# Performance work log

Hardware: AMD Instinct MI355X
Metric: run time of the kernel (lower is better)

## Reference

```python
import jax, jax.numpy as jnp
import numpy as np

LN_EPS = 1e-5  # torch.nn.LayerNorm default

def g(x):
    # minGRU activation: x + 0.5 for x >= 0, sigmoid(x) otherwise (always positive)
    return jnp.where(x >= 0, x + 0.5, jax.nn.sigmoid(x))

def log_g(x):
    return jnp.where(x >= 0, jnp.log(jax.nn.relu(x) + 0.5), -jax.nn.softplus(-x))

def layernorm(x, gamma, beta):
    mu = jnp.mean(x, axis=-1, keepdims=True)
    var = jnp.var(x, axis=-1, keepdims=True)
    return (x - mu) * jax.lax.rsqrt(var + LN_EPS) * gamma + beta

def mingru_scan(gate, hidden, h0):
    # gate, hidden: (B,S,D); h0: (B,1,D) positive
    # z = sigmoid(gate); h_t = (1-z_t)*h_{t-1} + z_t * g(hidden_t)
    # evaluated via Heinsen parallel scan in log space
    log_z = -jax.nn.softplus(-gate)          # log sigmoid(gate)
    log_coeffs = -jax.nn.softplus(gate)      # log(1 - sigmoid(gate))
    log_h0 = jnp.log(h0)                     # (B,1,D)
    log_tilde_h = log_g(hidden)
    a_star = jnp.cumsum(
        jnp.concatenate([jnp.zeros_like(log_h0), log_coeffs], axis=1), axis=1
    )                                        # (B,S+1,D)
    log_vals = jnp.concatenate([log_h0, log_z + log_tilde_h], axis=1) - a_star
    log_h = a_star + jax.lax.cumlogsumexp(log_vals, axis=1)
    return jnp.exp(log_h)[:, 1:]             # (B,S,D)

def setup_inputs() -> dict:
    key = jax.random.key(0)
    k1, k2 = jax.random.split(key)
    B, S, D, L = 8, 4096, 1024, 3
    x = jax.random.normal(k1, (B, S, D), dtype=jnp.float32)
    W = jax.random.normal(k2, (L, D, 2 * D), dtype=jnp.float32) * 0.02
    b = jnp.zeros((L, 2 * D), dtype=jnp.float32)
    ln_gamma = jnp.ones((L, D), dtype=jnp.float32)
    ln_beta = jnp.zeros((L, D), dtype=jnp.float32)
    return {"x": x, "ln_gamma": ln_gamma, "ln_beta": ln_beta, "W": W, "b": b}

def reference(x, ln_gamma, ln_beta, W, b):
    B, S, D = x.shape
    L = W.shape[0]
    inp = x
    next_hidden = []
    for l in range(L):
        h_prev = jnp.full((B, 1, D), 0.5, dtype=x.dtype)  # g(zeros) = 0.5
        xn = layernorm(inp, ln_gamma[l], ln_beta[l])
        gh = jnp.einsum('bsd,de->bse', xn, W[l]) + b[l]   # (B,S,2D)
        gate, hidden = jnp.split(gh, 2, axis=2)
        out = mingru_scan(gate, hidden, h_prev)
        next_hidden.append(out[:, -1:])
        out = out + inp  # residual (sizes equal -> identity res_align)
        inp = out
    return (out, *next_hidden)
```

## Files before the change

### kernel.cpp

```cpp
#include <hip/hip_runtime.h>

typedef unsigned short u16;
typedef unsigned int   u32;
typedef float  f32x2  __attribute__((ext_vector_type(2)));
typedef float  f32x4  __attribute__((ext_vector_type(4)));
typedef short  bf16x8 __attribute__((ext_vector_type(8)));
typedef u16    u16x4  __attribute__((ext_vector_type(4)));
typedef u32    u32x4  __attribute__((ext_vector_type(4)));

#define BQ 8
#define SQ 4096
#define DQ 1024
#define NQ 2048
#define MQ 32768
#define KQ 1024
#define CCH 64
#define TCH 64
#define NT 16

__device__ __forceinline__ float bf2f(u16 u){
  union { u32 i; float f; } v; v.i = ((u32)u) << 16; return v.f;
}
__device__ __forceinline__ u16 f2bf(float f){
  union { float f; u32 i; } v; v.f = f;
  u32 r = v.i + 0x7fffu + ((v.i >> 16) & 1u);
  return (u16)(r >> 16);
}

__device__ __forceinline__ void sig_ab(float gate, float hid, float& a, float& bv){
  float eg = __expf(gate);
  float a_ = __builtin_amdgcn_rcpf(1.f + eg);
  float z  = 1.f - a_;
  float eh = __expf(hid);
  float sg = eh * __builtin_amdgcn_rcpf(1.f + eh);
  float gval = (hid >= 0.f) ? (hid + 0.5f) : sg;
  a = a_; bv = z * gval;
}

__device__ __forceinline__ void gload_lds16(const u16* g, u16* l){
  __builtin_amdgcn_global_load_lds(
      (const __attribute__((address_space(1))) u32*)g,
      (__attribute__((address_space(3)))       u32*)l,
      16, 0, 0);
}

__global__ __launch_bounds__(256) void wt_cast(const float* __restrict__ W,
                                               u16* __restrict__ WT){
  __shared__ float t[64][65];
  const int l  = blockIdx.z;
  const int k0 = blockIdx.x << 6, n0 = blockIdx.y << 6;
  const float* Wl = W  + (size_t)l * KQ * NQ;
  u16*         Tl = WT + (size_t)l * NQ * KQ;
  const int c = threadIdx.x & 63, r4 = threadIdx.x >> 6;
  #pragma unroll
  for (int i = 0; i < 16; ++i){
    int r = i * 4 + r4;
    t[r][c] = Wl[(size_t)(k0 + r) * NQ + n0 + c];
  }
  __syncthreads();
  #pragma unroll
  for (int i = 0; i < 16; ++i){
    int r = i * 4 + r4;
    Tl[(size_t)(n0 + r) * KQ + k0 + c] = f2bf(t[c][r]);
  }
}

__global__ __launch_bounds__(256) void ln_cast(const float* __restrict__ x,
                                               const float* __restrict__ gamma,
                                               const float* __restrict__ beta,
                                               u16* __restrict__ xn){
  const size_t row = blockIdx.x;
  const int tid = threadIdx.x;
  f32x4 xv = *(const f32x4*)(x + row * DQ + tid * 4);
  float s  = xv[0] + xv[1] + xv[2] + xv[3];
  float s2 = xv[0]*xv[0] + xv[1]*xv[1] + xv[2]*xv[2] + xv[3]*xv[3];
  #pragma unroll
  for (int off = 32; off > 0; off >>= 1){
    s  += __shfl_down(s,  off);
    s2 += __shfl_down(s2, off);
  }
  __shared__ float red[8];
  const int wave = tid >> 6, lane = tid & 63;
  if (lane == 0){ red[wave] = s; red[4 + wave] = s2; }
  __syncthreads();
  s  = red[0] + red[1] + red[2] + red[3];
  s2 = red[4] + red[5] + red[6] + red[7];
  const float mean = s * (1.f / DQ);
  float var = fmaxf(s2 * (1.f / DQ) - mean * mean, 0.f);
  const float rstd = rsqrtf(var + 1e-5f);
  f32x4 gv = *(const f32x4*)(gamma + tid * 4);
  f32x4 bv = *(const f32x4*)(beta  + tid * 4);
  u16x4 o;
  #pragma unroll
  for (int e = 0; e < 4; ++e) o[e] = f2bf((xv[e] - mean) * rstd * gv[e] + bv[e]);
  *(u16x4*)(xn + row * DQ + tid * 4) = o;
}

__global__ __launch_bounds__(512, 2) void gemm_k8(const u16* __restrict__ A,
                                                  const u16* __restrict__ Bt,
                                                  const float* __restrict__ bias,
                                                  u32* __restrict__ abv,
                                                  float* __restrict__ pq){
  __shared__ u16 lds[2][2][2][8192];
  const int bid = blockIdx.x;
  const int swz = ((bid & 7) << 7) | (bid >> 3);
  const int bn = swz & 7, bm = swz >> 3;
  const int m0 = bm << 8;
  const int tid = threadIdx.x;
  const int w = tid >> 6, lane = tid & 63;
  const int wr = w >> 2, wc = w & 3;
  const int lr = lane & 15, hi = lane >> 4;
  const int sl8 = lane >> 3;
  const int sslot = (lane & 7) ^ sl8;

  f32x4 acc[2][2][4][2] = {};
  bf16x8 afr[4][2];
  bf16x8 bf0[2][2], bf1[2][2];

#define FENCE asm volatile("" ::: "memory")
#define BAR do { FENCE; __builtin_amdgcn_s_barrier(); FENCE; } while(0)

#define STAGE(op, hf, kt, pb_) do {                                            \
    const u16* gsrc_ = (op) ? Bt : A;                                          \
    const int rb_ = (op) ? ((bn << 7) + (hf) * 1024) : (m0 + ((hf) << 7));     \
    _Pragma("unroll")                                                          \
    for (int g_ = 0; g_ < 2; ++g_){                                            \
      const int row_ = (w << 4) + (g_ << 3) + sl8;                             \
      gload_lds16(gsrc_ + (size_t)(rb_ + row_) * KQ + ((kt) << 6) + (sslot << 3),\
                  &lds[pb_][op][hf][((w << 4) + (g_ << 3)) << 6]);             \
    }                                                                          \
  } while(0)

#define LDSRD(dst, base_, row_, slot_) do {                                    \
    const int r_ = (row_);                                                     \
    dst = *(const bf16x8*)((const char*)(base_) +                              \
          ((r_ << 7) + ((((slot_)) ^ (r_ & 7)) << 4)));                        \
  } while(0)

#define RD_A(hf) do {                                                          \
    const u16* Ah_ = &lds[pb][0][hf][0];                                       \
    _Pragma("unroll")                                                          \
    for (int i_ = 0; i_ < 4; ++i_)                                             \
      _Pragma("unroll")                                                        \
      for (int kk_ = 0; kk_ < 2; ++kk_)                                        \
        LDSRD(afr[i_][kk_], Ah_, (wr << 6) + (i_ << 4) + lr, (kk_ << 2) + hi); \
  } while(0)

#define RD_B(dst, hf) do {                                                     \
    const u16* Bh_ = &lds[pb][1][hf][0];                                       \
    _Pragma("unroll")                                                          \
    for (int j_ = 0; j_ < 2; ++j_)                                             \
      _Pragma("unroll")                                                        \
      for (int kk_ = 0; kk_ < 2; ++kk_)                                        \
        LDSRD(dst[j_][kk_], Bh_, (wc << 5) + (j_ << 4) + lr, (kk_ << 2) + hi); \
  } while(0)

#define MM(qm, qn, B) do {                                                     \
    _Pragma("unroll")                                                          \
    for (int i_ = 0; i_ < 4; ++i_)                                             \
      _Pragma("unroll")                                                        \
      for (int j_ = 0; j_ < 2; ++j_)                                           \
        _Pragma("unroll")                                                      \
        for (int kk_ = 0; kk_ < 2; ++kk_)                                      \
          acc[qm][qn][i_][j_] = __builtin_amdgcn_mfma_f32_16x16x32_bf16(       \
              afr[i_][kk_], B[j_][kk_], acc[qm][qn][i_][j_], 0, 0, 0);         \
  } while(0)

#define PH(VMW, STG, RDS, MFMAS) do {                                          \
    VMW;                                                                       \
    BAR;                                                                       \
    STG;                                                                       \
    RDS;                                                                       \
    asm volatile("s_waitcnt lgkmcnt(0)" ::: "memory");                         \
    __builtin_amdgcn_s_setprio(1);                                             \
    MFMAS;                                                                     \
    __builtin_amdgcn_s_setprio(0);                                             \
  } while(0)

  STAGE(1, 0, 0, 0); STAGE(0, 0, 0, 0); STAGE(1, 1, 0, 0); STAGE(0, 1, 0, 0);

  for (int t = 0; t < NT; ++t){
    const int pb = t & 1, qb = pb ^ 1;
    const bool s = (t + 1 < NT);
    PH(asm volatile("s_waitcnt vmcnt(4)" ::: "memory"),
       if (s) STAGE(1, 0, t + 1, qb),
       RD_A(0); RD_B(bf0, 0),
       MM(0, 0, bf0));
    PH(if (s) { asm volatile("s_waitcnt vmcnt(4)" ::: "memory"); }
       else   { asm volatile("s_waitcnt vmcnt(2)" ::: "memory"); },
       if (s) STAGE(0, 0, t + 1, qb),
       RD_B(bf1, 1),
       MM(0, 1, bf1));
    PH(if (s) { asm volatile("s_waitcnt vmcnt(4)" ::: "memory"); }
       else   { asm volatile("s_waitcnt vmcnt(0)" ::: "memory"); },
       if (s) STAGE(1, 1, t + 1, qb),
       RD_A(1),
       MM(1, 0, bf0));
    PH(,
       if (s) STAGE(0, 1, t + 1, qb),
       ,
       MM(1, 1, bf1));
  }
#undef PH
#undef MM
#undef RD_B
#undef RD_A
#undef LDSRD
#undef STAGE

  const int dbase = (bn << 7) + (wc << 5) + lr;
  #pragma unroll
  for (int qm = 0; qm < 2; ++qm){
    const int row00 = m0 + (qm << 7) + (wr << 6);
    float chP[2] = {1.f, 1.f}, chQ[2] = {0.f, 0.f};
    #pragma unroll
    for (int i = 0; i < 4; ++i){
      float sgP[2] = {1.f, 1.f}, sgQ[2] = {0.f, 0.f};
      #pragma unroll
      for (int r = 0; r < 4; ++r){
        const int row = row00 + (i << 4) + (hi << 2) + r;
        #pragma unroll
        for (int j = 0; j < 2; ++j){
          const int d = dbase + (j << 4);
          float gate = acc[qm][0][i][j][r] + bias[d];
          float hid  = acc[qm][1][i][j][r] + bias[1024 + d];
          float a, bv; sig_ab(gate, hid, a, bv);
          const u16 ua = f2bf(a), ub = f2bf(bv);
          abv[(size_t)row * 1024 + d] = (u32)ua | ((u32)ub << 16);
          const float ar = bf2f(ua), br = bf2f(ub);
          sgQ[j] = ar * sgQ[j] + br;
          sgP[j] *= ar;
        }
      }
      #pragma unroll
      for (int j = 0; j < 2; ++j){
        float p = sgP[j], q = sgQ[j];
        float p1 = __shfl_up(p, 16), q1 = __shfl_up(q, 16);
        if (hi >= 1){ q = p * q1 + q; p = p * p1; }
        float p2 = __shfl_up(p, 32), q2 = __shfl_up(q, 32);
        if (hi >= 2){ q = p * q2 + q; p = p * p2; }
        chQ[j] = p * chQ[j] + q;
        chP[j] = p * chP[j];
      }
    }
    if (hi == 3){
      const int bq = row00 >> 12, cq = (row00 >> 6) & 63;
      #pragma unroll
      for (int j = 0; j < 2; ++j){
        const int d = dbase + (j << 4);
        f32x2 v; v[0] = chP[j]; v[1] = chQ[j];
        *(f32x2*)(pq + ((((size_t)(bq * CCH + cq)) << 10) + d) * 2) = v;
      }
    }
  }
#undef BAR
#undef FENCE
}

__global__ __launch_bounds__(256) void scan2(const float* __restrict__ pq,
                                             float* __restrict__ hst,
                                             float* __restrict__ hlast){
  const int idx = blockIdx.x * 256 + threadIdx.x;
  const int b = idx >> 10, d = idx & 1023;
  float h = 0.5f;
  for (int c = 0; c < CCH; ++c){
    const size_t o = ((size_t)(b * CCH + c) << 10) + d;
    hst[o] = h;
    f32x2 v = *(const f32x2*)(pq + o * 2);
    h = v[0] * h + v[1];
  }
  hlast[idx] = h;
}

template<int MODE>
__global__ __launch_bounds__(256) void scan3f(const u32* __restrict__ abv,
                                              const float* __restrict__ hst,
                                              const void* __restrict__ inp,
                                              void* __restrict__ outp,
                                              u16* __restrict__ xn,
                                              const float* __restrict__ gamma,
                                              const float* __restrict__ beta){
  const int b = blockIdx.x >> 6;
  const int c = blockIdx.x & 63;
  const int tid = threadIdx.x;
  const int d4 = tid << 2;
  const int wave = tid >> 6, lane = tid & 63;
  const size_t srow = (size_t)(b * SQ + c * TCH);
  const u32* base = abv + srow * 1024 + d4;
  const size_t o = ((size_t)blockIdx.x << 10) + d4;
  f32x4 h0v = *(const f32x4*)(hst + o);
  float h[4] = {h0v[0], h0v[1], h0v[2], h0v[3]};
  __shared__ float red[2][8];
  f32x4 gv = {}, bvv = {};
  if (MODE != 2){
    gv  = *(const f32x4*)(gamma + d4);
    bvv = *(const f32x4*)(beta  + d4);
  }
  for (int t = 0; t < TCH; ++t){
    u32x4 ab = *(const u32x4*)(base + (size_t)t * 1024);
    f32x4 iv;
    if (MODE == 0){
      iv = *(const f32x4*)((const float*)inp + (srow + t) * DQ + d4);
    } else {
      u16x4 ib = *(const u16x4*)((const u16*)inp + (srow + t) * DQ + d4);
      #pragma unroll
      for (int e = 0; e < 4; ++e) iv[e] = bf2f(ib[e]);
    }
    f32x4 ov;
    #pragma unroll
    for (int e = 0; e < 4; ++e){
      const float a  = bf2f((u16)(ab[e] & 0xffffu));
      const float bv = bf2f((u16)(ab[e] >> 16));
      h[e] = a * h[e] + bv;
      ov[e] = h[e] + iv[e];
    }
    if (MODE == 2){
      *(f32x4*)((float*)outp + (srow + t) * DQ + d4) = ov;
    } else {
      u16x4 ob;
      #pragma unroll
      for (int e = 0; e < 4; ++e) ob[e] = f2bf(ov[e]);
      *(u16x4*)((u16*)outp + (srow + t) * DQ + d4) = ob;
      float s  = ov[0] + ov[1] + ov[2] + ov[3];
      float s2 = ov[0]*ov[0] + ov[1]*ov[1] + ov[2]*ov[2] + ov[3]*ov[3];
      #pragma unroll
      for (int off = 32; off > 0; off >>= 1){
        s  += __shfl_down(s,  off);
        s2 += __shfl_down(s2, off);
      }
      const int rb = t & 1;
      if (lane == 0){ red[rb][wave] = s; red[rb][4 + wave] = s2; }
      __syncthreads();
      s  = red[rb][0] + red[rb][1] + red[rb][2] + red[rb][3];
      s2 = red[rb][4] + red[rb][5] + red[rb][6] + red[rb][7];
      const float mean = s * (1.f / DQ);
      float var = fmaxf(s2 * (1.f / DQ) - mean * mean, 0.f);
      const float rstd = rsqrtf(var + 1e-5f);
      u16x4 xo;
      #pragma unroll
      for (int e = 0; e < 4; ++e)
        xo[e] = f2bf((ov[e] - mean) * rstd * gv[e] + bvv[e]);
      *(u16x4*)(xn + (srow + t) * DQ + d4) = xo;
    }
  }
}

extern "C" void kernel_launch(void* const* d_in, const int* in_sizes, int n_in,
                              void* d_out, int out_size, void* d_ws, size_t ws_size,
                              hipStream_t stream) {
  const float* x     = (const float*)d_in[0];
  const float* gamma = (const float*)d_in[1];
  const float* beta  = (const float*)d_in[2];
  const float* W     = (const float*)d_in[3];
  const float* bias  = (const float*)d_in[4];
  float* out = (float*)d_out;

  char* ws = (char*)d_ws;
  const size_t ACT = (size_t)MQ * DQ * 4;
  u16*   bufA = (u16*)(ws);
  u16*   bufB = (u16*)(ws + ACT);
  u32*   abv  = (u32*)(ws + 2 * ACT);
  u16*   xn   = (u16*)(ws + 3 * ACT);
  u16*   WT   = (u16*)(ws + 3 * ACT + (size_t)MQ * DQ * 2);
  float* pq   = (float*)(ws + 3 * ACT + (size_t)MQ * DQ * 2 + (size_t)3 * NQ * KQ * 2);
  float* hst  = pq + (size_t)2 * BQ * CCH * DQ;

  wt_cast<<<dim3(KQ / 64, NQ / 64, 3), 256, 0, stream>>>(W, WT);

  const dim3 ggrid((NQ / 256) * (MQ / 256));
  ln_cast<<<MQ, 256, 0, stream>>>(x, gamma, beta, xn);
  gemm_k8<<<ggrid, 512, 0, stream>>>(xn, WT, bias, abv, pq);
  scan2<<<(BQ * DQ) / 256, 256, 0, stream>>>(pq, hst, out + (size_t)MQ * DQ);
  scan3f<0><<<BQ * CCH, 256, 0, stream>>>(abv, hst, x, bufA, xn,
                                          gamma + DQ, beta + DQ);
  gemm_k8<<<ggrid, 512, 0, stream>>>(xn, WT + (size_t)NQ * KQ, bias + NQ,
                                     abv, pq);
  scan2<<<(BQ * DQ) / 256, 256, 0, stream>>>(pq, hst,
                                             out + (size_t)MQ * DQ + BQ * DQ);
  scan3f<1><<<BQ * CCH, 256, 0, stream>>>(abv, hst, bufA, bufB, xn,
                                          gamma + 2 * DQ, beta + 2 * DQ);
  gemm_k8<<<ggrid, 512, 0, stream>>>(xn, WT + (size_t)2 * NQ * KQ, bias + 2 * NQ,
                                     abv, pq);
  scan2<<<(BQ * DQ) / 256, 256, 0, stream>>>(pq, hst,
                                             out + (size_t)MQ * DQ + 2 * BQ * DQ);
  scan3f<2><<<BQ * CCH, 256, 0, stream>>>(abv, hst, bufB, out, nullptr,
                                          nullptr, nullptr);
}
```

Measured before the change: 732.5 us.

## Software-pipeline LDS fragment reads with MFMA using double-buffered A registers

```diff
diff --git a/kernel.cpp b/kernel.cpp
--- a/kernel.cpp
+++ b/kernel.cpp
@@ -114,11 +114,12 @@
   const int sslot = (lane & 7) ^ sl8;
 
   f32x4 acc[2][2][4][2] = {};
-  bf16x8 afr[4][2];
+  bf16x8 afrA[4][2], afrB[4][2];
   bf16x8 bf0[2][2], bf1[2][2];
 
 #define FENCE asm volatile("" ::: "memory")
 #define BAR do { FENCE; __builtin_amdgcn_s_barrier(); FENCE; } while(0)
+#define SB  __builtin_amdgcn_sched_barrier(0)
 
 #define STAGE(op, hf, kt, pb_) do {                                            \
     const u16* gsrc_ = (op) ? Bt : A;                                          \
@@ -137,17 +138,17 @@
           ((r_ << 7) + ((((slot_)) ^ (r_ & 7)) << 4)));                        \
   } while(0)
 
-#define RD_A(hf) do {                                                          \
-    const u16* Ah_ = &lds[pb][0][hf][0];                                       \
+#define RD_A(dst, hf, buf_) do {                                               \
+    const u16* Ah_ = &lds[buf_][0][hf][0];                                     \
     _Pragma("unroll")                                                          \
     for (int i_ = 0; i_ < 4; ++i_)                                             \
       _Pragma("unroll")                                                        \
       for (int kk_ = 0; kk_ < 2; ++kk_)                                        \
-        LDSRD(afr[i_][kk_], Ah_, (wr << 6) + (i_ << 4) + lr, (kk_ << 2) + hi); \
-  } while(0)
-
-#define RD_B(dst, hf) do {                                                     \
-    const u16* Bh_ = &lds[pb][1][hf][0];                                       \
+        LDSRD(dst[i_][kk_], Ah_, (wr << 6) + (i_ << 4) + lr, (kk_ << 2) + hi); \
+  } while(0)
+
+#define RD_B(dst, hf, buf_) do {                                               \
+    const u16* Bh_ = &lds[buf_][1][hf][0];                                     \
     _Pragma("unroll")                                                          \
     for (int j_ = 0; j_ < 2; ++j_)                                             \
       _Pragma("unroll")                                                        \
@@ -155,7 +156,9 @@
         LDSRD(dst[j_][kk_], Bh_, (wc << 5) + (j_ << 4) + lr, (kk_ << 2) + hi); \
   } while(0)
 
-#define MM(qm, qn, B) do {                                                     \
+#define MM(qm, qn, AR, B) do {                                                 \
+    SB;                                                                        \
+    __builtin_amdgcn_s_setprio(1);                                             \
     _Pragma("unroll")                                                          \
     for (int i_ = 0; i_ < 4; ++i_)                                             \
       _Pragma("unroll")                                                        \
@@ -163,50 +166,45 @@
         _Pragma("unroll")                                                      \
         for (int kk_ = 0; kk_ < 2; ++kk_)                                      \
           acc[qm][qn][i_][j_] = __builtin_amdgcn_mfma_f32_16x16x32_bf16(       \
-              afr[i_][kk_], B[j_][kk_], acc[qm][qn][i_][j_], 0, 0, 0);         \
-  } while(0)
-
-#define PH(VMW, STG, RDS, MFMAS) do {                                          \
-    VMW;                                                                       \
-    BAR;                                                                       \
-    STG;                                                                       \
-    RDS;                                                                       \
-    asm volatile("s_waitcnt lgkmcnt(0)" ::: "memory");                         \
-    __builtin_amdgcn_s_setprio(1);                                             \
-    MFMAS;                                                                     \
+              AR[i_][kk_], B[j_][kk_], acc[qm][qn][i_][j_], 0, 0, 0);          \
     __builtin_amdgcn_s_setprio(0);                                             \
   } while(0)
 
   STAGE(1, 0, 0, 0); STAGE(0, 0, 0, 0); STAGE(1, 1, 0, 0); STAGE(0, 1, 0, 0);
+  asm volatile("s_waitcnt vmcnt(4)" ::: "memory");
+  BAR;
+  RD_A(afrA, 0, 0); RD_B(bf0, 0, 0);
 
   for (int t = 0; t < NT; ++t){
     const int pb = t & 1, qb = pb ^ 1;
     const bool s = (t + 1 < NT);
-    PH(asm volatile("s_waitcnt vmcnt(4)" ::: "memory"),
-       if (s) STAGE(1, 0, t + 1, qb),
-       RD_A(0); RD_B(bf0, 0),
-       MM(0, 0, bf0));
-    PH(if (s) { asm volatile("s_waitcnt vmcnt(4)" ::: "memory"); }
-       else   { asm volatile("s_waitcnt vmcnt(2)" ::: "memory"); },
-       if (s) STAGE(0, 0, t + 1, qb),
-       RD_B(bf1, 1),
-       MM(0, 1, bf1));
-    PH(if (s) { asm volatile("s_waitcnt vmcnt(4)" ::: "memory"); }
-       else   { asm volatile("s_waitcnt vmcnt(0)" ::: "memory"); },
-       if (s) STAGE(1, 1, t + 1, qb),
-       RD_A(1),
-       MM(1, 0, bf0));
-    PH(,
-       if (s) STAGE(0, 1, t + 1, qb),
-       ,
-       MM(1, 1, bf1));
-  }
-#undef PH
+    asm volatile("s_waitcnt vmcnt(2)" ::: "memory");
+    BAR;
+    if (s) STAGE(1, 0, t + 1, qb);
+    RD_B(bf1, 1, pb);
+    MM(0, 0, afrA, bf0);
+    if (s) { asm volatile("s_waitcnt vmcnt(2)" ::: "memory"); }
+    else   { asm volatile("s_waitcnt vmcnt(0)" ::: "memory"); }
+    BAR;
+    if (s) STAGE(0, 0, t + 1, qb);
+    RD_A(afrB, 1, pb);
+    MM(0, 1, afrA, bf1);
+    if (s) STAGE(1, 1, t + 1, qb);
+    MM(1, 0, afrB, bf0);
+    if (s){
+      asm volatile("s_waitcnt vmcnt(2)" ::: "memory");
+      BAR;
+      STAGE(0, 1, t + 1, qb);
+      RD_A(afrA, 0, qb); RD_B(bf0, 0, qb);
+    }
+    MM(1, 1, afrB, bf1);
+  }
 #undef MM
 #undef RD_B
 #undef RD_A
 #undef LDSRD
 #undef STAGE
+#undef SB
 
   const int dbase = (bn << 7) + (wc << 5) + lr;
   #pragma unroll
```

Measured after the change: 746.2 us. Within noise of the previous version (+1.9%).
